# Kernel optimization log

Measured on AMD Instinct MI355X. Metric: run time of the kernel, lower is better.

Reference implementation:

```python
import jax, jax.numpy as jnp
import numpy as np

N_NODES = 100000
N_EDGES = 1600000
D_FEAT = 48


def setup_inputs() -> dict:
    key = jax.random.key(0)
    k1, k2, k3, k4 = jax.random.split(key, 4)
    rows = jax.random.randint(k1, (N_EDGES,), 0, N_NODES, dtype=jnp.int32)
    cols = jax.random.randint(k2, (N_EDGES,), 0, N_NODES, dtype=jnp.int32)
    # normalized adjacency values (positive, like D^-1/2 A D^-1/2 entries)
    vals = jax.random.uniform(k3, (N_EDGES,), dtype=jnp.float32)
    embeds = jax.random.normal(k4, (N_NODES, D_FEAT), dtype=jnp.float32)
    return {"rows": rows, "cols": cols, "vals": vals, "embeds": embeds}


def reference(rows, cols, vals, embeds):
    # torch.spmm(adj, embeds) with adj in COO form:
    # out[i] = sum_{e : rows[e]==i} vals[e] * embeds[cols[e]]
    msgs = vals[:, None] * embeds[cols]          # [E, D] gather + scale
    out = jax.ops.segment_sum(msgs, rows, num_segments=embeds.shape[0])  # [N, D]
    return out
```

## Files before the change

### kernel.cpp

```cpp
#include <hip/hip_runtime.h>


#define N_NODES 100000
#define D_FEAT 48
#define DQ (D_FEAT / 4)

#define BUCKET_BITS 7
#define BUCKET_NODES 128
#define N_BUCKETS ((N_NODES + BUCKET_NODES - 1) / BUCKET_NODES)
#define CAPB 2432

#define CHUNK 8192
#define P1_THREADS 1024
#define VPT (CHUNK / P1_THREADS / 4)

#define P2_THREADS 512
#define EPT2 ((CAPB + P2_THREADS - 1) / P2_THREADS)
#define NG (P2_THREADS / 12)

#define OVF_CAP 4096
#define EBF_UINT2 (N_NODES * DQ)

typedef float  fl32x4 __attribute__((ext_vector_type(4)));
typedef unsigned long long u64;

__device__ __forceinline__ unsigned short f2bf(float f) {
    unsigned u = __float_as_uint(f);
    return (unsigned short)((u + 0x7FFFu + ((u >> 16) & 1u)) >> 16);
}

__device__ __forceinline__ float4 bf2f4(uint2 h) {
    float4 m;
    m.x = __uint_as_float((h.x & 0xFFFFu) << 16);
    m.y = __uint_as_float(h.x & 0xFFFF0000u);
    m.z = __uint_as_float((h.y & 0xFFFFu) << 16);
    m.w = __uint_as_float(h.y & 0xFFFF0000u);
    return m;
}

__global__ __launch_bounds__(P1_THREADS) void partition_kernel(
        const int* __restrict__ rows, const int* __restrict__ cols,
        const float* __restrict__ vals, int* __restrict__ gcur,
        uint2* __restrict__ tmp, uint4* __restrict__ ovf, int* __restrict__ novf,
        const float* __restrict__ embeds, uint2* __restrict__ ebf,
        int n_edges) {
    __shared__ int counts[N_BUCKETS];
    __shared__ int starts[N_BUCKETS];
    __shared__ int cursor[N_BUCKETS];
    __shared__ int adj[N_BUCKETS];
    __shared__ int wtot[16];
    __shared__ unsigned lkey[CHUNK];
    __shared__ unsigned lval[CHUNK];
    __shared__ int      ldst[CHUNK];

    int t = threadIdx.x;
    int lane = t & 63;
    int wid = t >> 6;
    int base = blockIdx.x * CHUNK;
    int n = min(CHUNK, n_edges - base);
    int n4 = n >> 2;

    for (int i = t; i < N_BUCKETS; i += P1_THREADS) counts[i] = 0;
    __syncthreads();

    int      b[VPT * 4];
    unsigned key[VPT * 4];
    float    v[VPT * 4];
    const int4*   rows4 = reinterpret_cast<const int4*>(rows + base);
    const int4*   cols4 = reinterpret_cast<const int4*>(cols + base);
    const float4* vals4 = reinterpret_cast<const float4*>(vals + base);
#pragma unroll
    for (int k = 0; k < VPT; ++k) {
        int idx4 = k * P1_THREADS + t;
        bool ok = idx4 < n4;
        int4   r4 = ok ? rows4[idx4] : make_int4(0, 0, 0, 0);
        int4   c4 = ok ? cols4[idx4] : make_int4(0, 0, 0, 0);
        float4 v4 = ok ? vals4[idx4] : make_float4(0.f, 0.f, 0.f, 0.f);
        int rr[4] = {r4.x, r4.y, r4.z, r4.w};
        int cc[4] = {c4.x, c4.y, c4.z, c4.w};
        float vv[4] = {v4.x, v4.y, v4.z, v4.w};
#pragma unroll
        for (int j = 0; j < 4; ++j) {
            int i = k * 4 + j;
            b[i] = -1;
            if (ok) {
                b[i] = rr[j] >> BUCKET_BITS;
                key[i] = ((unsigned)(rr[j] & (BUCKET_NODES - 1)) << 17) | (unsigned)cc[j];
                v[i] = vv[j];
                atomicAdd(&counts[b[i]], 1);
            }
        }
    }

    if (ebf) {
        const float4* e4 = reinterpret_cast<const float4*>(embeds);
        int stride = gridDim.x * P1_THREADS;
        for (int i = blockIdx.x * P1_THREADS + t; i < EBF_UINT2; i += stride) {
            float4 f = e4[i];
            uint2 p;
            p.x = (unsigned)f2bf(f.x) | ((unsigned)f2bf(f.y) << 16);
            p.y = (unsigned)f2bf(f.z) | ((unsigned)f2bf(f.w) << 16);
            ebf[i] = p;
        }
    }
    __syncthreads();

    int cnt_t = (t < N_BUCKETS) ? counts[t] : 0;
    int x = cnt_t;
#pragma unroll
    for (int d = 1; d < 64; d <<= 1) {
        int y = __shfl_up(x, d, 64);
        if (lane >= d) x += y;
    }
    if (lane == 63) wtot[wid] = x;
    __syncthreads();
    if (t < 64) {
        int w = (t < 16) ? wtot[t] : 0;
        int xs = w;
#pragma unroll
        for (int d = 1; d < 16; d <<= 1) {
            int y = __shfl_up(xs, d, 64);
            if (lane >= d) xs += y;
        }
        if (t < 16) wtot[t] = xs - w;
    }
    __syncthreads();
    if (t < N_BUCKETS) {
        int excl = x - cnt_t + wtot[wid];
        starts[t] = excl;
        cursor[t] = excl;
        int gp = (cnt_t > 0) ? atomicAdd(&gcur[t], cnt_t) : 0;
        adj[t] = t * CAPB + gp - excl;
    }
    __syncthreads();

#pragma unroll
    for (int i = 0; i < VPT * 4; ++i) {
        if (b[i] >= 0) {
            int p = atomicAdd(&cursor[b[i]], 1);
            int dest = adj[b[i]] + p;
            if (dest < (b[i] + 1) * CAPB) {
                lkey[p] = key[i];
                lval[p] = __float_as_uint(v[i]);
                ldst[p] = dest;
            } else {
                ldst[p] = -1;
                int o = atomicAdd(novf, 1);
                if (o < OVF_CAP) {
                    unsigned rl = key[i] >> 17;
                    ovf[o] = make_uint4((unsigned)b[i] * BUCKET_NODES + rl,
                                        key[i] & 0x1FFFFu, __float_as_uint(v[i]), 0u);
                }
            }
        }
    }
    __syncthreads();

    u64* tmp8 = reinterpret_cast<u64*>(tmp);
    for (int i = t; i < n; i += P1_THREADS) {
        int d = ldst[i];
        if (d >= 0)
            tmp8[d] = (u64)lkey[i] | ((u64)lval[i] << 32);
    }
}

#define ACCUM_OVF_TAIL(GATHER_EXPR)                                             \
    {                                                                           \
        int nov = min(*novf, OVF_CAP);                                          \
        if (nov > 0) {                                                          \
            __syncthreads();                                                    \
            int lo = bkt * BUCKET_NODES, hi = lo + BUCKET_NODES;                \
            for (int i = t; i < nov; i += P2_THREADS) {                         \
                uint4 en = ovf[i];                                              \
                int node = (int)en.x;                                           \
                if (node >= lo && node < hi && node < N_NODES) {                \
                    unsigned c = en.y;                                          \
                    float v = __uint_as_float(en.z);                            \
                    for (int qq = 0; qq < DQ; ++qq) {                           \
                        float4 m = GATHER_EXPR;                                 \
                        float* dst = out + (size_t)node * D_FEAT + qq * 4;      \
                        atomicAdd(dst + 0, v * m.x);                            \
                        atomicAdd(dst + 1, v * m.y);                            \
                        atomicAdd(dst + 2, v * m.z);                            \
                        atomicAdd(dst + 3, v * m.w);                            \
                    }                                                           \
                }                                                               \
            }                                                                   \
        }                                                                       \
    }

__global__ __launch_bounds__(P2_THREADS) void accum_bf16_kernel(
        const int* __restrict__ gcur, const uint2* __restrict__ tmp,
        const uint2* __restrict__ ebf, float* __restrict__ out,
        const int* __restrict__ novf, const uint4* __restrict__ ovf) {
    __shared__ uint2 sorted[CAPB];
    __shared__ int cnt[BUCKET_NODES];
    __shared__ int cur[BUCKET_NODES];
    __shared__ int roff[BUCKET_NODES + 1];
    __shared__ int ws2[2];

    int t = threadIdx.x;
    int lane = t & 63;
    int bkt = blockIdx.x;
    const uint2* bucket = tmp + (size_t)bkt * CAPB;
    int cntE = min(gcur[bkt], CAPB);

    if (t < BUCKET_NODES) cnt[t] = 0;
    __syncthreads();

    unsigned kcol[EPT2]; unsigned vbits[EPT2]; int erl[EPT2];
#pragma unroll
    for (int j = 0; j < EPT2; ++j) {
        int idx = t + j * P2_THREADS;
        erl[j] = -1;
        if (idx < cntE) {
            u64 pk8 = __builtin_nontemporal_load(
                reinterpret_cast<const u64*>(bucket) + idx);
            unsigned kx = (unsigned)pk8;
            erl[j] = (int)(kx >> 17);
            kcol[j] = kx & 0x1FFFFu;
            vbits[j] = (unsigned)(pk8 >> 32);
            atomicAdd(&cnt[erl[j]], 1);
        }
    }
    __syncthreads();

    int x = 0;
    if (t < BUCKET_NODES) {
        x = cnt[t];
#pragma unroll
        for (int d = 1; d < 64; d <<= 1) {
            int y = __shfl_up(x, d, 64);
            if (lane >= d) x += y;
        }
        if (lane == 63) ws2[t >> 6] = x;
    }
    __syncthreads();
    if (t == 0) { int a = ws2[0]; ws2[0] = 0; ws2[1] = a; }
    __syncthreads();
    if (t < BUCKET_NODES) {
        int incl = x + ws2[t >> 6];
        int st = incl - cnt[t];
        roff[t] = st; cur[t] = st;
    }
    if (t == 0) roff[BUCKET_NODES] = cntE;
    __syncthreads();

#pragma unroll
    for (int j = 0; j < EPT2; ++j) {
        if (erl[j] >= 0) {
            int pos = atomicAdd(&cur[erl[j]], 1);
            sorted[pos] = make_uint2(kcol[j], vbits[j]);
        }
    }
    __syncthreads();

    int g = t / 12, q = t - g * 12;
    if (g < NG) {
        const uint2* ebq = ebf + q;
        for (int rl = g; rl < BUCKET_NODES; rl += NG) {
            int e = roff[rl], e1 = roff[rl + 1];
            float4 a = make_float4(0.f, 0.f, 0.f, 0.f);
            for (; e + 3 < e1; e += 4) {
                uint2 p0 = sorted[e],     p1 = sorted[e + 1];
                uint2 p2 = sorted[e + 2], p3 = sorted[e + 3];
                uint2 h0 = ebq[p0.x * DQ];
                uint2 h1 = ebq[p1.x * DQ];
                uint2 h2 = ebq[p2.x * DQ];
                uint2 h3 = ebq[p3.x * DQ];
                float v0 = __uint_as_float(p0.y), v1 = __uint_as_float(p1.y);
                float v2 = __uint_as_float(p2.y), v3 = __uint_as_float(p3.y);
                float4 m0 = bf2f4(h0), m1 = bf2f4(h1);
                float4 m2 = bf2f4(h2), m3 = bf2f4(h3);
                a.x += v0 * m0.x; a.y += v0 * m0.y; a.z += v0 * m0.z; a.w += v0 * m0.w;
                a.x += v1 * m1.x; a.y += v1 * m1.y; a.z += v1 * m1.z; a.w += v1 * m1.w;
                a.x += v2 * m2.x; a.y += v2 * m2.y; a.z += v2 * m2.z; a.w += v2 * m2.w;
                a.x += v3 * m3.x; a.y += v3 * m3.y; a.z += v3 * m3.z; a.w += v3 * m3.w;
            }
            for (; e < e1; ++e) {
                uint2 p0 = sorted[e];
                float4 m0 = bf2f4(ebq[p0.x * DQ]);
                float v0 = __uint_as_float(p0.y);
                a.x += v0 * m0.x; a.y += v0 * m0.y; a.z += v0 * m0.z; a.w += v0 * m0.w;
            }
            int node = bkt * BUCKET_NODES + rl;
            if (node < N_NODES) {
                fl32x4 av = {a.x, a.y, a.z, a.w};
                __builtin_nontemporal_store(
                    av, reinterpret_cast<fl32x4*>(out + (size_t)node * D_FEAT) + q);
            }
        }
    }
    ACCUM_OVF_TAIL(bf2f4(ebf[c * DQ + qq]))
}

__global__ __launch_bounds__(P2_THREADS) void accum_f32_kernel(
        const int* __restrict__ gcur, const uint2* __restrict__ tmp,
        const float* __restrict__ embeds, float* __restrict__ out,
        const int* __restrict__ novf, const uint4* __restrict__ ovf) {
    __shared__ uint2 sorted[CAPB];
    __shared__ int cnt[BUCKET_NODES];
    __shared__ int cur[BUCKET_NODES];
    __shared__ int roff[BUCKET_NODES + 1];
    __shared__ int ws2[2];
    int t = threadIdx.x;
    int lane = t & 63;
    int bkt = blockIdx.x;
    const uint2* bucket = tmp + (size_t)bkt * CAPB;
    int cntE = min(gcur[bkt], CAPB);
    if (t < BUCKET_NODES) cnt[t] = 0;
    __syncthreads();
    unsigned kcol[EPT2]; unsigned vbits[EPT2]; int erl[EPT2];
#pragma unroll
    for (int j = 0; j < EPT2; ++j) {
        int idx = t + j * P2_THREADS;
        erl[j] = -1;
        if (idx < cntE) {
            uint2 pk = bucket[idx];
            erl[j] = (int)(pk.x >> 17);
            kcol[j] = pk.x & 0x1FFFFu;
            vbits[j] = pk.y;
            atomicAdd(&cnt[erl[j]], 1);
        }
    }
    __syncthreads();
    int x = 0;
    if (t < BUCKET_NODES) {
        x = cnt[t];
#pragma unroll
        for (int d = 1; d < 64; d <<= 1) {
            int y = __shfl_up(x, d, 64);
            if (lane >= d) x += y;
        }
        if (lane == 63) ws2[t >> 6] = x;
    }
    __syncthreads();
    if (t == 0) { int a = ws2[0]; ws2[0] = 0; ws2[1] = a; }
    __syncthreads();
    if (t < BUCKET_NODES) {
        int incl = x + ws2[t >> 6];
        int st = incl - cnt[t];
        roff[t] = st; cur[t] = st;
    }
    if (t == 0) roff[BUCKET_NODES] = cntE;
    __syncthreads();
#pragma unroll
    for (int j = 0; j < EPT2; ++j) {
        if (erl[j] >= 0) {
            int p = atomicAdd(&cur[erl[j]], 1);
            sorted[p] = make_uint2(kcol[j], vbits[j]);
        }
    }
    __syncthreads();
    int g = t / 12;
    int q = t - g * 12;
    if (g < NG) {
        for (int rl = g; rl < BUCKET_NODES; rl += NG) {
            int s = roff[rl], epos = roff[rl + 1];
            float4 a0 = make_float4(0.f, 0.f, 0.f, 0.f);
            int e = s;
            for (; e < epos; ++e) {
                uint2 p0 = sorted[e];
                float4 m0 = *(reinterpret_cast<const float4*>(embeds + p0.x * D_FEAT) + q);
                float v0 = __uint_as_float(p0.y);
                a0.x += v0 * m0.x; a0.y += v0 * m0.y; a0.z += v0 * m0.z; a0.w += v0 * m0.w;
            }
            int node = bkt * BUCKET_NODES + rl;
            if (node < N_NODES)
                *(reinterpret_cast<float4*>(out + (size_t)node * D_FEAT) + q) = a0;
        }
    }
    ACCUM_OVF_TAIL((*(reinterpret_cast<const float4*>(embeds + (size_t)c * D_FEAT) + qq)))
}

extern "C" void kernel_launch(void* const* d_in, const int* in_sizes, int n_in,
                              void* d_out, int out_size, void* d_ws, size_t ws_size,
                              hipStream_t stream) {
    const int*   rows   = (const int*)d_in[0];
    const int*   cols   = (const int*)d_in[1];
    const float* vals   = (const float*)d_in[2];
    const float* embeds = (const float*)d_in[3];
    float*       out    = (float*)d_out;
    int n_edges = in_sizes[0];

    const size_t TMP_OFF = 4096 + 65536;
    const size_t TMP_SZ  = (size_t)N_BUCKETS * CAPB * sizeof(uint2);
    const size_t EBF_OFF = TMP_OFF + TMP_SZ;
    const size_t EBF_SZ  = (size_t)EBF_UINT2 * sizeof(uint2);
    char* ws = (char*)d_ws;
    int*   gcur = (int*)(ws);
    int*   novf = (int*)(ws + 3200);
    uint4* ovf  = (uint4*)(ws + 4096);
    uint2* tmp  = (uint2*)(ws + TMP_OFF);
    uint2* ebf  = (uint2*)(ws + EBF_OFF);

    bool use_bf16 = ws_size >= EBF_OFF + EBF_SZ;

    hipMemsetAsync(ws, 0, 3264, stream);

    int p1_blocks = (n_edges + CHUNK - 1) / CHUNK;
    partition_kernel<<<p1_blocks, P1_THREADS, 0, stream>>>(
        rows, cols, vals, gcur, tmp, ovf, novf,
        embeds, use_bf16 ? ebf : (uint2*)nullptr, n_edges);

    if (use_bf16)
        accum_bf16_kernel<<<N_BUCKETS, P2_THREADS, 0, stream>>>(gcur, tmp, ebf, out, novf, ovf);
    else
        accum_f32_kernel<<<N_BUCKETS, P2_THREADS, 0, stream>>>(gcur, tmp, embeds, out, novf, ovf);
}
```

Before: 133.7 us.

## Use 768-thread blocks with 6 lanes per node and 16-byte bf16 gathers

The accumulation phase now runs 768 threads per bucket, so each of the 128 nodes gets exactly six lanes. Each lane loads eight bf16 features (a uint4) per edge instead of four, halving the number of gather loads per edge and removing the strided node loop. The cost is more threads per block, with fewer registers available per thread and lower occupancy. The f32 fallback kernel also gets larger blocks through the shared P2_THREADS.

```diff
diff --git a/kernel.cpp b/kernel.cpp
--- a/kernel.cpp
+++ b/kernel.cpp
@@ -4,6 +4,7 @@
 #define N_NODES 100000
 #define D_FEAT 48
 #define DQ (D_FEAT / 4)
+#define DQ4 (D_FEAT / 8)
 
 #define BUCKET_BITS 7
 #define BUCKET_NODES 128
@@ -14,9 +15,9 @@
 #define P1_THREADS 1024
 #define VPT (CHUNK / P1_THREADS / 4)
 
-#define P2_THREADS 512
+#define P2_THREADS 768
 #define EPT2 ((CAPB + P2_THREADS - 1) / P2_THREADS)
-#define NG (P2_THREADS / 12)
+#define NG6 (P2_THREADS / 6)
 
 #define OVF_CAP 4096
 #define EBF_UINT2 (N_NODES * DQ)
@@ -255,40 +256,50 @@
     }
     __syncthreads();
 
-    int g = t / 12, q = t - g * 12;
-    if (g < NG) {
-        const uint2* ebq = ebf + q;
-        for (int rl = g; rl < BUCKET_NODES; rl += NG) {
-            int e = roff[rl], e1 = roff[rl + 1];
-            float4 a = make_float4(0.f, 0.f, 0.f, 0.f);
-            for (; e + 3 < e1; e += 4) {
-                uint2 p0 = sorted[e],     p1 = sorted[e + 1];
-                uint2 p2 = sorted[e + 2], p3 = sorted[e + 3];
-                uint2 h0 = ebq[p0.x * DQ];
-                uint2 h1 = ebq[p1.x * DQ];
-                uint2 h2 = ebq[p2.x * DQ];
-                uint2 h3 = ebq[p3.x * DQ];
-                float v0 = __uint_as_float(p0.y), v1 = __uint_as_float(p1.y);
-                float v2 = __uint_as_float(p2.y), v3 = __uint_as_float(p3.y);
-                float4 m0 = bf2f4(h0), m1 = bf2f4(h1);
-                float4 m2 = bf2f4(h2), m3 = bf2f4(h3);
-                a.x += v0 * m0.x; a.y += v0 * m0.y; a.z += v0 * m0.z; a.w += v0 * m0.w;
-                a.x += v1 * m1.x; a.y += v1 * m1.y; a.z += v1 * m1.z; a.w += v1 * m1.w;
-                a.x += v2 * m2.x; a.y += v2 * m2.y; a.z += v2 * m2.z; a.w += v2 * m2.w;
-                a.x += v3 * m3.x; a.y += v3 * m3.y; a.z += v3 * m3.z; a.w += v3 * m3.w;
-            }
-            for (; e < e1; ++e) {
-                uint2 p0 = sorted[e];
-                float4 m0 = bf2f4(ebq[p0.x * DQ]);
-                float v0 = __uint_as_float(p0.y);
-                a.x += v0 * m0.x; a.y += v0 * m0.y; a.z += v0 * m0.z; a.w += v0 * m0.w;
-            }
-            int node = bkt * BUCKET_NODES + rl;
-            if (node < N_NODES) {
-                fl32x4 av = {a.x, a.y, a.z, a.w};
-                __builtin_nontemporal_store(
-                    av, reinterpret_cast<fl32x4*>(out + (size_t)node * D_FEAT) + q);
-            }
+    int g = t / 6, q = t - g * 6;
+    {
+        const uint4* ebq = reinterpret_cast<const uint4*>(ebf) + q;
+        int rl = g;
+        int e = roff[rl], e1 = roff[rl + 1];
+        float4 aA = make_float4(0.f, 0.f, 0.f, 0.f);
+        float4 aB = make_float4(0.f, 0.f, 0.f, 0.f);
+        for (; e + 3 < e1; e += 4) {
+            uint2 p0 = sorted[e],     p1 = sorted[e + 1];
+            uint2 p2 = sorted[e + 2], p3 = sorted[e + 3];
+            uint4 h0 = ebq[p0.x * DQ4];
+            uint4 h1 = ebq[p1.x * DQ4];
+            uint4 h2 = ebq[p2.x * DQ4];
+            uint4 h3 = ebq[p3.x * DQ4];
+            float v0 = __uint_as_float(p0.y), v1 = __uint_as_float(p1.y);
+            float v2 = __uint_as_float(p2.y), v3 = __uint_as_float(p3.y);
+            float4 mA0 = bf2f4(make_uint2(h0.x, h0.y)), mB0 = bf2f4(make_uint2(h0.z, h0.w));
+            float4 mA1 = bf2f4(make_uint2(h1.x, h1.y)), mB1 = bf2f4(make_uint2(h1.z, h1.w));
+            float4 mA2 = bf2f4(make_uint2(h2.x, h2.y)), mB2 = bf2f4(make_uint2(h2.z, h2.w));
+            float4 mA3 = bf2f4(make_uint2(h3.x, h3.y)), mB3 = bf2f4(make_uint2(h3.z, h3.w));
+            aA.x += v0 * mA0.x; aA.y += v0 * mA0.y; aA.z += v0 * mA0.z; aA.w += v0 * mA0.w;
+            aB.x += v0 * mB0.x; aB.y += v0 * mB0.y; aB.z += v0 * mB0.z; aB.w += v0 * mB0.w;
+            aA.x += v1 * mA1.x; aA.y += v1 * mA1.y; aA.z += v1 * mA1.z; aA.w += v1 * mA1.w;
+            aB.x += v1 * mB1.x; aB.y += v1 * mB1.y; aB.z += v1 * mB1.z; aB.w += v1 * mB1.w;
+            aA.x += v2 * mA2.x; aA.y += v2 * mA2.y; aA.z += v2 * mA2.z; aA.w += v2 * mA2.w;
+            aB.x += v2 * mB2.x; aB.y += v2 * mB2.y; aB.z += v2 * mB2.z; aB.w += v2 * mB2.w;
+            aA.x += v3 * mA3.x; aA.y += v3 * mA3.y; aA.z += v3 * mA3.z; aA.w += v3 * mA3.w;
+            aB.x += v3 * mB3.x; aB.y += v3 * mB3.y; aB.z += v3 * mB3.z; aB.w += v3 * mB3.w;
+        }
+        for (; e < e1; ++e) {
+            uint2 p0 = sorted[e];
+            uint4 h0 = ebq[p0.x * DQ4];
+            float v0 = __uint_as_float(p0.y);
+            float4 mA0 = bf2f4(make_uint2(h0.x, h0.y)), mB0 = bf2f4(make_uint2(h0.z, h0.w));
+            aA.x += v0 * mA0.x; aA.y += v0 * mA0.y; aA.z += v0 * mA0.z; aA.w += v0 * mA0.w;
+            aB.x += v0 * mB0.x; aB.y += v0 * mB0.y; aB.z += v0 * mB0.z; aB.w += v0 * mB0.w;
+        }
+        int node = bkt * BUCKET_NODES + rl;
+        if (node < N_NODES) {
+            float* dst = out + (size_t)node * D_FEAT + q * 8;
+            fl32x4 A = {aA.x, aA.y, aA.z, aA.w};
+            fl32x4 B = {aB.x, aB.y, aB.z, aB.w};
+            __builtin_nontemporal_store(A, reinterpret_cast<fl32x4*>(dst));
+            __builtin_nontemporal_store(B, reinterpret_cast<fl32x4*>(dst + 4));
         }
     }
     ACCUM_OVF_TAIL(bf2f4(ebf[c * DQ + qq]))
@@ -354,8 +365,8 @@
     __syncthreads();
     int g = t / 12;
     int q = t - g * 12;
-    if (g < NG) {
-        for (int rl = g; rl < BUCKET_NODES; rl += NG) {
+    if (g < P2_THREADS / 12) {
+        for (int rl = g; rl < BUCKET_NODES; rl += P2_THREADS / 12) {
             int s = roff[rl], epos = roff[rl + 1];
             float4 a0 = make_float4(0.f, 0.f, 0.f, 0.f);
             int e = s;
```

New measurement: 132.2 us. About the same (-1.1%).
